# Performance work log

Measured on AMD Instinct MI355X. Metric: run time of the kernel, lower is better.

## Reference

```python
import jax, jax.numpy as jnp
import numpy as np


def setup_inputs() -> dict:
    key = jax.random.key(0)
    k1, k2, k3 = jax.random.split(key, 3)
    bs, chart_len, H = 256, 1024, 256
    num_steps, start_index = 512, 512
    chart = jax.random.normal(k1, (bs, chart_len, 2 * H), dtype=jnp.float32)
    operations = jax.random.randint(k2, (num_steps, bs, 2), 0, start_index, dtype=jnp.int64)
    U = jax.random.normal(k3, (5 * H, 2 * H), dtype=jnp.float32) * 0.05
    b = jnp.zeros((5 * H,), dtype=jnp.float32)
    return {"chart": chart, "operations": operations, "start_index": start_index, "U": U, "b": b}


def reference(chart, operations, start_index, U, b):
    H = U.shape[0] // 5
    bs = chart.shape[0]
    batch_idx = jnp.arange(bs)
    num_steps = operations.shape[0]

    def step_fn(ch, xs):
        step, ops = xs
        left = ch[batch_idx, ops[:, 0]]   # [bs, 2H]
        right = ch[batch_idx, ops[:, 1]]  # [bs, 2H]
        ccL, ccR = left[:, :H], right[:, :H]
        hh = jnp.concatenate([left[:, H:], right[:, H:]], axis=-1)  # [bs, 2H]
        preact = hh @ U.T + b  # [bs, 5H]
        i = jax.nn.sigmoid(preact[:, :H])
        fL = jax.nn.sigmoid(preact[:, H:2 * H])
        fR = jax.nn.sigmoid(preact[:, 2 * H:3 * H])
        o = jax.nn.sigmoid(preact[:, 3 * H:4 * H])
        u = jnp.tanh(preact[:, 4 * H:5 * H])
        c = fL * ccL + fR * ccR + i * u
        h = o * jnp.tanh(c)
        ch = ch.at[:, start_index + step, :].set(jnp.concatenate([c, h], axis=-1))
        return ch, None

    chart, _ = jax.lax.scan(step_fn, chart, (jnp.arange(num_steps), operations))
    return chart
```

## Files before the change

kernel.cpp:

```cpp
#include <hip/hip_runtime.h>
#include <hip/hip_bf16.h>

#define H_     256
#define TWOH_  512
#define CL_    1024
#define BS_    256
#define START_ 512

#define BM_   64
#define BK_   64
#define AKP_  72
#define BKP_  72
#define NCOL_ 320

typedef float  f32x16  __attribute__((ext_vector_type(16)));
typedef short  short8_t __attribute__((ext_vector_type(8)));
typedef short  short4_t __attribute__((ext_vector_type(4)));
typedef __bf16 bf16x8  __attribute__((ext_vector_type(8)));

static __device__ __forceinline__ unsigned short f2bf(float x) {
  __hip_bfloat16 h = __float2bfloat16(x);
  return __builtin_bit_cast(unsigned short, h);
}

__global__ void uconv_kernel(const float* __restrict__ U,
                             unsigned short* __restrict__ ub) {
  int tid = blockIdx.x * 256 + threadIdx.x;
  if (tid >= 1280 * 512) return;
  int n = tid >> 9, k = tid & 511;
  int g = n >> 8, j = n & 255;
  int jc = j >> 6, c = (g << 6) + (j & 63);
  ub[((jc * 320 + c) << 9) + k] = f2bf(U[tid]);
}

__global__ void copy_kernel(const float4* __restrict__ src,
                            float4* __restrict__ dst) {
  long long tid = (long long)blockIdx.x * blockDim.x + threadIdx.x;
  const long long total = 16777216LL;
  for (long long e = tid; e < total; e += (long long)gridDim.x * blockDim.x) {
    long long i   = e >> 16;
    long long rem = e & 65535;
    long long off = (i << 17) + rem;
    dst[off] = src[off];
  }
}

template<int USE_WS>
__global__ __launch_bounds__(256, 2) void chart_kernel(
    const float* __restrict__ chart,
    const int* __restrict__ ops,
    const float* __restrict__ U,
    const unsigned short* __restrict__ ub,
    const float* __restrict__ bias,
    float* __restrict__ out)
{
  __shared__ unsigned short As[BM_ * AKP_];
  __shared__ unsigned short Bs[NCOL_ * BKP_];
  __shared__ int opsl[2 * BM_];

  const int tid  = threadIdx.x;
  const int lane = tid & 63;
  const int wid  = tid >> 6;
  const int wm   = wid & 1;
  const int wn   = wid >> 1;

  const int bx    = blockIdx.x;
  const int jc    = blockIdx.y;
  const int s     = bx >> 2;
  const int ibase = (bx & 3) * BM_;
  const int j0    = jc * 64;

  if (tid < 2 * BM_) opsl[tid] = ops[(s * BS_ + ibase) * 2 + tid];
  __syncthreads();

  const int arow = tid >> 2;
  const int aqc  = tid & 3;
  const int opL_s = opsl[2 * arow];
  const int opR_s = opsl[2 * arow + 1];
  const long long abase_i = (long long)(ibase + arow) * CL_;

  f32x16 acc[5];
  #pragma unroll
  for (int g = 0; g < 5; ++g)
    #pragma unroll
    for (int q = 0; q < 16; ++q) acc[g][q] = 0.0f;

  const int a_off  = (wm * 32 + (lane & 31)) * AKP_ + 8 * (lane >> 5);
  const int b_off0 = (wn * 32 + (lane & 31)) * BKP_ + 8 * (lane >> 5);

  for (int kt = 0; kt < 8; ++kt) {
    const int k0 = kt * BK_;
    {
      const int op   = (k0 < 256) ? opL_s : opR_s;
      const int col0 = ((k0 < 256) ? 256 + k0 : k0) + aqc * 16;
      const float* src = chart + (abase_i + op) * TWOH_ + col0;
      float4 f0 = *(const float4*)(src + 0);
      float4 f1 = *(const float4*)(src + 4);
      float4 f2 = *(const float4*)(src + 8);
      float4 f3 = *(const float4*)(src + 12);
      short8_t v0, v1;
      v0[0] = (short)f2bf(f0.x); v0[1] = (short)f2bf(f0.y);
      v0[2] = (short)f2bf(f0.z); v0[3] = (short)f2bf(f0.w);
      v0[4] = (short)f2bf(f1.x); v0[5] = (short)f2bf(f1.y);
      v0[6] = (short)f2bf(f1.z); v0[7] = (short)f2bf(f1.w);
      v1[0] = (short)f2bf(f2.x); v1[1] = (short)f2bf(f2.y);
      v1[2] = (short)f2bf(f2.z); v1[3] = (short)f2bf(f2.w);
      v1[4] = (short)f2bf(f3.x); v1[5] = (short)f2bf(f3.y);
      v1[6] = (short)f2bf(f3.z); v1[7] = (short)f2bf(f3.w);
      *(short8_t*)&As[arow * AKP_ + aqc * 16]     = v0;
      *(short8_t*)&As[arow * AKP_ + aqc * 16 + 8] = v1;
    }
    if constexpr (USE_WS) {
      #pragma unroll
      for (int cc = 0; cc < 10; ++cc) {
        int chunk = cc * 256 + tid;
        int c  = chunk >> 3;
        int ko = (chunk & 7) * 8;
        short8_t v = *(const short8_t*)(ub + ((jc * 320 + c) << 9) + k0 + ko);
        *(short8_t*)&Bs[c * BKP_ + ko] = v;
      }
    } else {
      #pragma unroll
      for (int cc = 0; cc < 20; ++cc) {
        int chunk = cc * 256 + tid;
        int c  = chunk >> 4;
        int ko = (chunk & 15) * 4;
        int n  = ((c >> 6) << 8) + j0 + (c & 63);
        float4 f = *(const float4*)(U + (long long)n * 512 + k0 + ko);
        short4_t v;
        v[0] = (short)f2bf(f.x); v[1] = (short)f2bf(f.y);
        v[2] = (short)f2bf(f.z); v[3] = (short)f2bf(f.w);
        *(short4_t*)&Bs[c * BKP_ + ko] = v;
      }
    }
    __syncthreads();

    #pragma unroll
    for (int ks = 0; ks < 4; ++ks) {
      bf16x8 a = __builtin_bit_cast(bf16x8, *(const short8_t*)&As[a_off + ks * 16]);
      #pragma unroll
      for (int g = 0; g < 5; ++g) {
        bf16x8 b = __builtin_bit_cast(bf16x8,
            *(const short8_t*)&Bs[b_off0 + g * 64 * BKP_ + ks * 16]);
        acc[g] = __builtin_amdgcn_mfma_f32_32x32x16_bf16(a, b, acc[g], 0, 0, 0);
      }
    }
    __syncthreads();
  }

  const int jlane = j0 + wn * 32 + (lane & 31);
  float bg[5];
  #pragma unroll
  for (int g = 0; g < 5; ++g) bg[g] = bias[g * H_ + jlane];

  #pragma unroll
  for (int q = 0; q < 16; ++q) {
    int rl  = wm * 32 + (q & 3) + 8 * (q >> 2) + 4 * (lane >> 5);
    int i   = ibase + rl;
    int opL = opsl[2 * rl], opR = opsl[2 * rl + 1];
    float ccL = chart[((long long)i * CL_ + opL) * TWOH_ + jlane];
    float ccR = chart[((long long)i * CL_ + opR) * TWOH_ + jlane];
    float pi  = acc[0][q] + bg[0];
    float pfL = acc[1][q] + bg[1];
    float pfR = acc[2][q] + bg[2];
    float po  = acc[3][q] + bg[3];
    float pu  = acc[4][q] + bg[4];
    float gi  = 1.f / (1.f + __expf(-pi));
    float gfL = 1.f / (1.f + __expf(-pfL));
    float gfR = 1.f / (1.f + __expf(-pfR));
    float go  = 1.f / (1.f + __expf(-po));
    float eu  = __expf(2.f * pu);
    float gu  = 1.f - 2.f / (eu + 1.f);
    float c   = gfL * ccL + gfR * ccR + gi * gu;
    float ec  = __expf(2.f * c);
    float th  = 1.f - 2.f / (ec + 1.f);
    float h   = go * th;
    float* orow = out + ((long long)i * CL_ + START_ + s) * TWOH_;
    orow[jlane]      = c;
    orow[H_ + jlane] = h;
  }
}

extern "C" void kernel_launch(void* const* d_in, const int* in_sizes, int n_in,
                              void* d_out, int out_size, void* d_ws, size_t ws_size,
                              hipStream_t stream) {
  const float* chart = (const float*)d_in[0];
  const int*   ops   = (const int*)d_in[1];
  const float* U     = (const float*)d_in[3];
  const float* bias  = (const float*)d_in[4];
  float* out = (float*)d_out;

  copy_kernel<<<4096, 256, 0, stream>>>((const float4*)chart, (float4*)out);

  const size_t ub_bytes = (size_t)1280 * 512 * 2;
  if (ws_size >= ub_bytes) {
    unsigned short* ub = (unsigned short*)d_ws;
    uconv_kernel<<<2560, 256, 0, stream>>>(U, ub);
    chart_kernel<1><<<dim3(2048, 4), 256, 0, stream>>>(chart, ops, U, ub, bias, out);
  } else {
    chart_kernel<0><<<dim3(2048, 4), 256, 0, stream>>>(chart, ops, U, nullptr, bias, out);
  }
}
```

Measured before the change: 470.3 us.

## Pre-convert chart hidden states to bf16 and double-buffer async LDS loads

Adds a pre-pass that converts the hidden half of the chart's first 512 positions to bf16 in workspace. The main kernel then gathers operands via global_load_lds directly into XOR-swizzled, double-buffered shared memory, using 128-row tiles with two accumulator sets per wave. This is meant to halve gather bytes, overlap loads with MFMA, and cut conversion work in the inner loop. In exchange it costs an extra full pass over the chart and 64 MB more workspace, and falls back to the old kernel when the workspace is too small.

```diff
diff --git a/kernel.cpp b/kernel.cpp
--- a/kernel.cpp
+++ b/kernel.cpp
@@ -7,20 +7,20 @@
 #define BS_    256
 #define START_ 512
 
-#define BM_   64
-#define BK_   64
-#define AKP_  72
-#define BKP_  72
-#define NCOL_ 320
-
-typedef float  f32x16  __attribute__((ext_vector_type(16)));
+typedef float  f32x16   __attribute__((ext_vector_type(16)));
 typedef short  short8_t __attribute__((ext_vector_type(8)));
 typedef short  short4_t __attribute__((ext_vector_type(4)));
-typedef __bf16 bf16x8  __attribute__((ext_vector_type(8)));
+typedef __bf16 bf16x8   __attribute__((ext_vector_type(8)));
 
 static __device__ __forceinline__ unsigned short f2bf(float x) {
   __hip_bfloat16 h = __float2bfloat16(x);
   return __builtin_bit_cast(unsigned short, h);
+}
+
+static __device__ __forceinline__ void gload16(const void* g, void* l) {
+  __builtin_amdgcn_global_load_lds(
+      (const __attribute__((address_space(1))) void*)g,
+      (__attribute__((address_space(3))) void*)l, 16, 0, 0);
 }
 
 __global__ void uconv_kernel(const float* __restrict__ U,
@@ -31,6 +31,23 @@
   int g = n >> 8, j = n & 255;
   int jc = j >> 6, c = (g << 6) + (j & 63);
   ub[((jc * 320 + c) << 9) + k] = f2bf(U[tid]);
+}
+
+__global__ void hbconv_kernel(const float* __restrict__ chart,
+                              unsigned short* __restrict__ hb) {
+  size_t t = (size_t)blockIdx.x * 256 + threadIdx.x;
+  size_t row = t >> 5;
+  int    kc  = (int)(t & 31) * 8;
+  size_t i = row >> 9, pos = row & 511;
+  const float* src = chart + (i * CL_ + pos) * TWOH_ + H_ + kc;
+  float4 f0 = *(const float4*)(src);
+  float4 f1 = *(const float4*)(src + 4);
+  short8_t v;
+  v[0] = (short)f2bf(f0.x); v[1] = (short)f2bf(f0.y);
+  v[2] = (short)f2bf(f0.z); v[3] = (short)f2bf(f0.w);
+  v[4] = (short)f2bf(f1.x); v[5] = (short)f2bf(f1.y);
+  v[6] = (short)f2bf(f1.z); v[7] = (short)f2bf(f1.w);
+  *(short8_t*)(hb + row * H_ + kc) = v;
 }
 
 __global__ void copy_kernel(const float4* __restrict__ src,
@@ -45,38 +62,157 @@
   }
 }
 
-template<int USE_WS>
-__global__ __launch_bounds__(256, 2) void chart_kernel(
+__global__ __launch_bounds__(256, 2) void chart2_kernel(
+    const float* __restrict__ chart,
+    const int* __restrict__ ops,
+    const unsigned short* __restrict__ ub,
+    const unsigned short* __restrict__ hb,
+    const float* __restrict__ bias,
+    float* __restrict__ out)
+{
+  __shared__ unsigned short As[2][128 * 32];
+  __shared__ unsigned short Bs[2][320 * 32];
+  __shared__ int opsl[256];
+
+  const int tid = threadIdx.x, lane = tid & 63, wid = tid >> 6;
+  const int l31 = lane & 31, lhi = lane >> 5;
+  const int wm = wid & 1, wn = wid >> 1;
+  const int bx = blockIdx.x, jc = blockIdx.y;
+  const int s = bx >> 1, ibase = (bx & 1) * 128;
+
+  opsl[tid] = ops[(s * BS_ + ibase) * 2 + tid];
+  __syncthreads();
+
+  int rA[2], opAL[2], opAR[2], csA[2];
+  #pragma unroll
+  for (int q = 0; q < 2; ++q) {
+    rA[q]   = (wid * 2 + q) * 16 + (lane >> 2);
+    opAL[q] = opsl[2 * rA[q]];
+    opAR[q] = opsl[2 * rA[q] + 1];
+    csA[q]  = (((lane & 3) ^ ((rA[q] >> 1) & 3))) * 8;
+  }
+  int rB[5], csB[5];
+  #pragma unroll
+  for (int p = 0; p < 5; ++p) {
+    rB[p]  = (wid * 5 + p) * 16 + (lane >> 2);
+    csB[p] = (((lane & 3) ^ ((rB[p] >> 1) & 3))) * 8;
+  }
+  const size_t ub_base = ((size_t)jc * 320) << 9;
+
+  f32x16 acc0[5], acc1[5];
+  #pragma unroll
+  for (int g = 0; g < 5; ++g)
+    #pragma unroll
+    for (int q = 0; q < 16; ++q) { acc0[g][q] = 0.f; acc1[g][q] = 0.f; }
+
+#define STAGE(BUF, KT) do {                                                     \
+    const int  kt_   = (KT);                                                    \
+    const bool left_ = kt_ < 8;                                                 \
+    const int  koff_ = left_ ? kt_ * 32 : kt_ * 32 - 256;                       \
+    _Pragma("unroll")                                                           \
+    for (int q = 0; q < 2; ++q) {                                               \
+      int op_ = left_ ? opAL[q] : opAR[q];                                      \
+      const unsigned short* g_ =                                                \
+          hb + ((size_t)(ibase + rA[q]) * 512 + op_) * 256 + koff_ + csA[q];    \
+      gload16(g_, &As[BUF][(wid * 2 + q) * 512]);                               \
+    }                                                                           \
+    _Pragma("unroll")                                                           \
+    for (int p = 0; p < 5; ++p) {                                               \
+      const unsigned short* g_ =                                                \
+          ub + ub_base + ((size_t)rB[p] << 9) + kt_ * 32 + csB[p];              \
+      gload16(g_, &Bs[BUF][(wid * 5 + p) * 512]);                               \
+    }                                                                           \
+  } while (0)
+
+  STAGE(0, 0);
+  __syncthreads();
+
+  const int sw   = (l31 >> 1) & 3;
+  const int aro0 = (wm * 64 + l31) * 32;
+  const int aro1 = (wm * 64 + 32 + l31) * 32;
+  const int bro  = (wn * 32 + l31) * 32;
+
+  int cur = 0;
+  for (int kt = 0; kt < 16; ++kt) {
+    if (kt + 1 < 16) STAGE(cur ^ 1, kt + 1);
+    #pragma unroll
+    for (int ks = 0; ks < 2; ++ks) {
+      const int ce = ((ks * 2 + lhi) ^ sw) * 8;
+      bf16x8 a0 = __builtin_bit_cast(bf16x8, *(const short8_t*)&As[cur][aro0 + ce]);
+      bf16x8 a1 = __builtin_bit_cast(bf16x8, *(const short8_t*)&As[cur][aro1 + ce]);
+      #pragma unroll
+      for (int g = 0; g < 5; ++g) {
+        bf16x8 b = __builtin_bit_cast(bf16x8,
+            *(const short8_t*)&Bs[cur][bro + g * 2048 + ce]);
+        acc0[g] = __builtin_amdgcn_mfma_f32_32x32x16_bf16(a0, b, acc0[g], 0, 0, 0);
+        acc1[g] = __builtin_amdgcn_mfma_f32_32x32x16_bf16(a1, b, acc1[g], 0, 0, 0);
+      }
+    }
+    __syncthreads();
+    cur ^= 1;
+  }
+#undef STAGE
+
+  const int jlane = jc * 64 + wn * 32 + l31;
+  float bg[5];
+  #pragma unroll
+  for (int g = 0; g < 5; ++g) bg[g] = bias[g * H_ + jlane];
+
+#define EPI(ACC, M) do {                                                        \
+    _Pragma("unroll")                                                           \
+    for (int q = 0; q < 16; ++q) {                                              \
+      const int row_ = wm * 64 + (M) * 32 + (q & 3) + 8 * (q >> 2) + 4 * lhi;   \
+      const int i_   = ibase + row_;                                            \
+      const int opL_ = opsl[2 * row_], opR_ = opsl[2 * row_ + 1];               \
+      const float ccL_ = chart[((size_t)i_ * CL_ + opL_) * TWOH_ + jlane];      \
+      const float ccR_ = chart[((size_t)i_ * CL_ + opR_) * TWOH_ + jlane];      \
+      float pi_  = (ACC)[0][q] + bg[0];                                         \
+      float pfL_ = (ACC)[1][q] + bg[1];                                         \
+      float pfR_ = (ACC)[2][q] + bg[2];                                         \
+      float po_  = (ACC)[3][q] + bg[3];                                         \
+      float pu_  = (ACC)[4][q] + bg[4];                                         \
+      float gi_  = 1.f / (1.f + __expf(-pi_));                                  \
+      float gfL_ = 1.f / (1.f + __expf(-pfL_));                                 \
+      float gfR_ = 1.f / (1.f + __expf(-pfR_));                                 \
+      float go_  = 1.f / (1.f + __expf(-po_));                                  \
+      float eu_  = __expf(2.f * pu_);                                           \
+      float gu_  = 1.f - 2.f / (eu_ + 1.f);                                     \
+      float c_   = gfL_ * ccL_ + gfR_ * ccR_ + gi_ * gu_;                       \
+      float ec_  = __expf(2.f * c_);                                            \
+      float th_  = 1.f - 2.f / (ec_ + 1.f);                                     \
+      float h_   = go_ * th_;                                                   \
+      float* orow_ = out + ((size_t)i_ * CL_ + START_ + s) * TWOH_;             \
+      orow_[jlane]      = c_;                                                   \
+      orow_[H_ + jlane] = h_;                                                   \
+    }                                                                           \
+  } while (0)
+
+  EPI(acc0, 0);
+  EPI(acc1, 1);
+#undef EPI
+}
+
+__global__ __launch_bounds__(256, 2) void chart1_kernel(
     const float* __restrict__ chart,
     const int* __restrict__ ops,
     const float* __restrict__ U,
-    const unsigned short* __restrict__ ub,
     const float* __restrict__ bias,
     float* __restrict__ out)
 {
-  __shared__ unsigned short As[BM_ * AKP_];
-  __shared__ unsigned short Bs[NCOL_ * BKP_];
-  __shared__ int opsl[2 * BM_];
-
-  const int tid  = threadIdx.x;
-  const int lane = tid & 63;
-  const int wid  = tid >> 6;
-  const int wm   = wid & 1;
-  const int wn   = wid >> 1;
-
-  const int bx    = blockIdx.x;
-  const int jc    = blockIdx.y;
-  const int s     = bx >> 2;
-  const int ibase = (bx & 3) * BM_;
-  const int j0    = jc * 64;
-
-  if (tid < 2 * BM_) opsl[tid] = ops[(s * BS_ + ibase) * 2 + tid];
+  __shared__ unsigned short As[64 * 72];
+  __shared__ unsigned short Bs[320 * 72];
+  __shared__ int opsl[128];
+
+  const int tid = threadIdx.x, lane = tid & 63, wid = tid >> 6;
+  const int wm = wid & 1, wn = wid >> 1;
+  const int bx = blockIdx.x, jc = blockIdx.y;
+  const int s = bx >> 2, ibase = (bx & 3) * 64, j0 = jc * 64;
+
+  if (tid < 128) opsl[tid] = ops[(s * BS_ + ibase) * 2 + tid];
   __syncthreads();
 
-  const int arow = tid >> 2;
-  const int aqc  = tid & 3;
-  const int opL_s = opsl[2 * arow];
-  const int opR_s = opsl[2 * arow + 1];
+  const int arow = tid >> 2, aqc = tid & 3;
+  const int opL_s = opsl[2 * arow], opR_s = opsl[2 * arow + 1];
   const long long abase_i = (long long)(ibase + arow) * CL_;
 
   f32x16 acc[5];
@@ -85,11 +221,11 @@
     #pragma unroll
     for (int q = 0; q < 16; ++q) acc[g][q] = 0.0f;
 
-  const int a_off  = (wm * 32 + (lane & 31)) * AKP_ + 8 * (lane >> 5);
-  const int b_off0 = (wn * 32 + (lane & 31)) * BKP_ + 8 * (lane >> 5);
+  const int a_off  = (wm * 32 + (lane & 31)) * 72 + 8 * (lane >> 5);
+  const int b_off0 = (wn * 32 + (lane & 31)) * 72 + 8 * (lane >> 5);
 
   for (int kt = 0; kt < 8; ++kt) {
-    const int k0 = kt * BK_;
+    const int k0 = kt * 64;
     {
       const int op   = (k0 < 256) ? opL_s : opR_s;
       const int col0 = ((k0 < 256) ? 256 + k0 : k0) + aqc * 16;
@@ -107,31 +243,20 @@
       v1[2] = (short)f2bf(f2.z); v1[3] = (short)f2bf(f2.w);
       v1[4] = (short)f2bf(f3.x); v1[5] = (short)f2bf(f3.y);
       v1[6] = (short)f2bf(f3.z); v1[7] = (short)f2bf(f3.w);
-      *(short8_t*)&As[arow * AKP_ + aqc * 16]     = v0;
-      *(short8_t*)&As[arow * AKP_ + aqc * 16 + 8] = v1;
+      *(short8_t*)&As[arow * 72 + aqc * 16]     = v0;
+      *(short8_t*)&As[arow * 72 + aqc * 16 + 8] = v1;
     }
-    if constexpr (USE_WS) {
-      #pragma unroll
-      for (int cc = 0; cc < 10; ++cc) {
-        int chunk = cc * 256 + tid;
-        int c  = chunk >> 3;
-        int ko = (chunk & 7) * 8;
-        short8_t v = *(const short8_t*)(ub + ((jc * 320 + c) << 9) + k0 + ko);
-        *(short8_t*)&Bs[c * BKP_ + ko] = v;
-      }
-    } else {
-      #pragma unroll
-      for (int cc = 0; cc < 20; ++cc) {
-        int chunk = cc * 256 + tid;
-        int c  = chunk >> 4;
-        int ko = (chunk & 15) * 4;
-        int n  = ((c >> 6) << 8) + j0 + (c & 63);
-        float4 f = *(const float4*)(U + (long long)n * 512 + k0 + ko);
-        short4_t v;
-        v[0] = (short)f2bf(f.x); v[1] = (short)f2bf(f.y);
-        v[2] = (short)f2bf(f.z); v[3] = (short)f2bf(f.w);
-        *(short4_t*)&Bs[c * BKP_ + ko] = v;
-      }
+    #pragma unroll
+    for (int cc = 0; cc < 20; ++cc) {
+      int chunk = cc * 256 + tid;
+      int c  = chunk >> 4;
+      int ko = (chunk & 15) * 4;
+      int n  = ((c >> 6) << 8) + j0 + (c & 63);
+      float4 f = *(const float4*)(U + (long long)n * 512 + k0 + ko);
+      short4_t v;
+      v[0] = (short)f2bf(f.x); v[1] = (short)f2bf(f.y);
+      v[2] = (short)f2bf(f.z); v[3] = (short)f2bf(f.w);
+      *(short4_t*)&Bs[c * 72 + ko] = v;
     }
     __syncthreads();
 
@@ -141,7 +266,7 @@
       #pragma unroll
       for (int g = 0; g < 5; ++g) {
         bf16x8 b = __builtin_bit_cast(bf16x8,
-            *(const short8_t*)&Bs[b_off0 + g * 64 * BKP_ + ks * 16]);
+            *(const short8_t*)&Bs[b_off0 + g * 64 * 72 + ks * 16]);
         acc[g] = __builtin_amdgcn_mfma_f32_32x32x16_bf16(a, b, acc[g], 0, 0, 0);
       }
     }
@@ -192,12 +317,18 @@
 
   copy_kernel<<<4096, 256, 0, stream>>>((const float4*)chart, (float4*)out);
 
-  const size_t ub_bytes = (size_t)1280 * 512 * 2;
-  if (ws_size >= ub_bytes) {
+  const size_t UB_BYTES = (size_t)1280 * 512 * 2;
+  const size_t HB_OFF   = (size_t)2 << 20;
+  const size_t HB_BYTES = (size_t)256 * 512 * 256 * 2;
+
+  if (ws_size >= HB_OFF + HB_BYTES) {
     unsigned short* ub = (unsigned short*)d_ws;
+    unsigned short* hb = (unsigned short*)((char*)d_ws + HB_OFF);
     uconv_kernel<<<2560, 256, 0, stream>>>(U, ub);
-    chart_kernel<1><<<dim3(2048, 4), 256, 0, stream>>>(chart, ops, U, ub, bias, out);
+    hbconv_kernel<<<16384, 256, 0, stream>>>(chart, hb);
+    chart2_kernel<<<dim3(1024, 4), 256, 0, stream>>>(chart, ops, ub, hb, bias, out);
   } else {
-    chart_kernel<0><<<dim3(2048, 4), 256, 0, stream>>>(chart, ops, U, nullptr, bias, out);
-  }
-}
+    chart1_kernel<<<dim3(2048, 4), 256, 0, stream>>>(chart, ops, U, bias, out);
+  }
+  (void)UB_BYTES;
+}
```

Measured after the change: 444.7 us. 1.06x faster.
